# Kernel optimization log

Hardware: AMD Instinct MI355X
Metric: run time of the kernel (lower is better)

Reference implementation:

```python
import jax, jax.numpy as jnp
import numpy as np

B, S, D = 4, 2048, 1024
H = 16
HD = D // H

def setup_inputs() -> dict:
    key = jax.random.key(0)
    ks = jax.random.split(key, 6)
    std = 1.0 / np.sqrt(D)
    x = jax.random.normal(ks[0], (B, S, D), dtype=jnp.float32)
    Wq = jax.random.uniform(ks[1], (D, D), jnp.float32, -std, std)
    Wk = jax.random.uniform(ks[2], (D, D), jnp.float32, -std, std)
    Wv = jax.random.uniform(ks[3], (D, D), jnp.float32, -std, std)
    Wo = jax.random.uniform(ks[4], (D, D), jnp.float32, -std, std)
    bo = jax.random.uniform(ks[5], (D,), jnp.float32, -std, std)
    return {"x": x, "Wq": Wq, "Wk": Wk, "Wv": Wv, "Wo": Wo, "bo": bo}

def reference(x, Wq, Wk, Wv, Wo, bo):
    b, s, _ = x.shape
    # projections; torch Linear computes x @ W^T, here W stored as (d_in, d_out)... we use (D, D) applied as x @ W
    q = (x @ Wq).reshape(b, s, H, HD).transpose(0, 2, 1, 3)  # b h s hd
    k = (x @ Wk).reshape(b, s, H, HD).transpose(0, 2, 1, 3)
    v = (x @ Wv).reshape(b, s, H, HD).transpose(0, 2, 1, 3)
    scores = jnp.einsum('bhqd,bhkd->bhqk', q, k)
    causal = jnp.triu(jnp.ones((s, s), dtype=bool), k=1)
    scores = jnp.where(causal[None, None], -jnp.inf, scores)
    attn = jax.nn.softmax(scores / np.sqrt(HD), axis=-1)  # dropout=0.0 -> identity
    ctx = jnp.einsum('bhqk,bhkd->bhqd', attn, v)
    ctx = ctx.transpose(0, 2, 1, 3).reshape(b, s, D)
    return ctx @ Wo + bo
```

## Files before the change

### kernel.cpp

```cpp
#include <hip/hip_runtime.h>

typedef unsigned short u16;
typedef __bf16 bf16x8 __attribute__((ext_vector_type(8)));
typedef float f32x4 __attribute__((ext_vector_type(4)));

#define Bn 4
#define Sn 2048
#define Dn 1024
#define Hn 16
#define HDn 64

__device__ inline u16 f2bf(float f) {
  unsigned u = __builtin_bit_cast(unsigned, f);
  u += 0x7fffu + ((u >> 16) & 1u);
  return (u16)(u >> 16);
}

__device__ __forceinline__ void gl2lds16(const u16* g, u16* l) {
  __builtin_amdgcn_global_load_lds(
      (const __attribute__((address_space(1))) unsigned int*)g,
      (__attribute__((address_space(3))) unsigned int*)l, 16, 0, 0);
}

__device__ __forceinline__ float fexp2(float x) {
  return __builtin_amdgcn_exp2f(x);
}

__device__ __forceinline__ unsigned pk_bf_trunc(float lo, float hi) {
  return __builtin_amdgcn_perm(__builtin_bit_cast(unsigned, hi),
                               __builtin_bit_cast(unsigned, lo), 0x07060302u);
}

__global__ __launch_bounds__(256) void cvt4(const float* __restrict__ in,
                                            u16* __restrict__ out, int n4) {
  int i = blockIdx.x * 256 + threadIdx.x;
  if (i < n4) {
    float4 v = ((const float4*)in)[i];
    ushort4 o;
    o.x = f2bf(v.x); o.y = f2bf(v.y); o.z = f2bf(v.z); o.w = f2bf(v.w);
    ((ushort4*)out)[i] = o;
  }
}

__global__ __launch_bounds__(256) void tcvt4(const float* __restrict__ w0,
                                             const float* __restrict__ w1,
                                             const float* __restrict__ w2,
                                             const float* __restrict__ w3,
                                             u16* __restrict__ out) {
  __shared__ u16 tile[32][33];
  const float* in = (blockIdx.z == 0) ? w0 : (blockIdx.z == 1) ? w1
                   : (blockIdx.z == 2) ? w2 : w3;
  u16* dst = out + (size_t)blockIdx.z * Dn * Dn;
  int bx = blockIdx.x * 32;
  int by = blockIdx.y * 32;
  int tx = threadIdx.x & 31;
  int ty = threadIdx.x >> 5;
#pragma unroll
  for (int r = 0; r < 32; r += 8)
    tile[ty + r][tx] = f2bf(in[(size_t)(by + ty + r) * Dn + bx + tx]);
  __syncthreads();
#pragma unroll
  for (int r = 0; r < 32; r += 8)
    dst[(size_t)(bx + ty + r) * Dn + by + tx] = tile[tx][ty + r];
}

__global__ __launch_bounds__(512, 2) void gemm_qkv(const u16* __restrict__ A,
                                                   const u16* __restrict__ Bt,
                                                   u16* __restrict__ qkb,
                                                   u16* __restrict__ vt,
                                                   float qscale) {
  __shared__ __attribute__((aligned(16))) u16 S[3][3][8192];

  const int tid = threadIdx.x;
  const int lane = tid & 63;
  const int lcol = lane & 15;
  const int quad = lane >> 4;
  const int wave = tid >> 6;
  const int wr = wave >> 2;
  const int wc = wave & 3;

  const int bid = blockIdx.x;
  const int idx = bid >> 3;
  const int bm = (((bid & 7) << 3) + (idx & 7)) * 128;
  const int bn = (idx >> 3) * 256;

  const u16* srcp[3][2];
#pragma unroll
  for (int rg = 0; rg < 3; rg++) {
#pragma unroll
    for (int j = 0; j < 2; j++) {
      int o = j * 8192 + tid * 16;
      int l = o ^ (((o >> 8) & 7) << 4);
      int rho = l >> 7;
      int c2 = (l >> 1) & 63;
      int gr;
      if (rg == 0)      gr = bm + rho;
      else if (rg == 1) gr = bn + ((rho >> 5) << 6) + (rho & 31);
      else              gr = bn + ((rho >> 5) << 6) + 32 + (rho & 31);
      const u16* base = (rg == 0) ? A : Bt;
      srcp[rg][j] = base + (size_t)gr * Dn + c2;
    }
  }

  auto stg = [&](int rg, int buf, int tile) {
    if (tile >= 16) return;
    const int k0 = tile << 6;
    u16* d = &S[buf][rg][tid * 8];
    gl2lds16(srcp[rg][0] + k0, d);
    gl2lds16(srcp[rg][1] + k0, d + 4096);
  };

  f32x4 acc[4][4];
#pragma unroll
  for (int i = 0; i < 4; i++)
#pragma unroll
    for (int j = 0; j < 4; j++) acc[i][j] = (f32x4){0.f, 0.f, 0.f, 0.f};

  const int SW = (lcol & 14) << 3;
  const int cs0 = (quad * 16) ^ SW;
  const int cs1 = (64 + quad * 16) ^ SW;

  bf16x8 bk0[4], bk1[4];

#define MFMA16(a, b, c) __builtin_amdgcn_mfma_f32_16x16x32_bf16(a, b, c, 0, 0, 0)

#define ARD(D, Q, F, K)                                                      \
  (*(const bf16x8*)((const char*)&S[D][0][0] +                               \
      ((wr * 64 + (Q) * 32 + (F) * 16 + lcol) * 128 + ((K) ? cs1 : cs0))))
#define BRD(D, NI, K)                                                        \
  (*(const bf16x8*)((const char*)&S[D][1 + ((NI) >> 1)][0] +                 \
      ((wc * 32 + ((NI) & 1) * 16 + lcol) * 128 + ((K) ? cs1 : cs0))))

#define PHASE(D, Q, DO_B, STG_STMT, WAIT_STMT)                               \
  {                                                                          \
    bf16x8 a00 = ARD(D, Q, 0, 0), a01 = ARD(D, Q, 0, 1);                     \
    bf16x8 a10 = ARD(D, Q, 1, 0), a11 = ARD(D, Q, 1, 1);                     \
    if (DO_B) {                                                              \
      _Pragma("unroll") for (int ni = 0; ni < 4; ni++) {                     \
        bk0[ni] = BRD(D, ni, 0);                                             \
        bk1[ni] = BRD(D, ni, 1);                                             \
      }                                                                      \
    }                                                                        \
    STG_STMT;                                                                \
    WAIT_STMT;                                                               \
    __builtin_amdgcn_s_barrier();                                            \
    asm volatile("s_waitcnt lgkmcnt(0)" ::: "memory");                       \
    __builtin_amdgcn_sched_barrier(0);                                       \
    __builtin_amdgcn_s_setprio(1);                                           \
    _Pragma("unroll") for (int ni = 0; ni < 4; ni++) {                       \
      acc[(Q) * 2][ni] = MFMA16(a00, bk0[ni], acc[(Q) * 2][ni]);             \
      acc[(Q) * 2][ni] = MFMA16(a01, bk1[ni], acc[(Q) * 2][ni]);             \
      acc[(Q) * 2 + 1][ni] = MFMA16(a10, bk0[ni], acc[(Q) * 2 + 1][ni]);     \
      acc[(Q) * 2 + 1][ni] = MFMA16(a11, bk1[ni], acc[(Q) * 2 + 1][ni]);     \
    }                                                                        \
    __builtin_amdgcn_s_setprio(0);                                           \
    __builtin_amdgcn_s_barrier();                                            \
  }

#define TILE(D, DN, T)                                                       \
  PHASE(D, 0, 1, { stg(1, DN, (T) + 2); stg(0, DN, (T) + 2); }, )            \
  PHASE(D, 1, 0, { stg(2, DN, (T) + 2); },                                   \
        if ((T) < 14) asm volatile("s_waitcnt vmcnt(6)" ::: "memory");       \
        else if ((T) == 14) asm volatile("s_waitcnt vmcnt(0)" ::: "memory"))

  stg(1, 0, 0); stg(0, 0, 0); stg(2, 0, 0);
  stg(1, 1, 1); stg(0, 1, 1); stg(2, 1, 1);
  asm volatile("s_waitcnt vmcnt(6)" ::: "memory");
  __builtin_amdgcn_s_barrier();

#pragma unroll 1
  for (int I = 0; I < 5; ++I) {
    const int T0 = 3 * I;
    TILE(0, 2, T0)
    TILE(1, 0, T0 + 1)
    TILE(2, 1, T0 + 2)
  }
  TILE(0, 2, 15)
#undef TILE
#undef PHASE
#undef ARD
#undef BRD
#undef MFMA16

  const int rb = bm + wr * 64 + quad * 4;
  const int cb = bn + wc * 64 + lcol;
  if (bn >= 2048) {
#pragma unroll
    for (int mi = 0; mi < 4; mi++) {
#pragma unroll
      for (int ni = 0; ni < 4; ni++) {
        int row0 = rb + mi * 16;
        int s = row0 & (Sn - 1);
        int bb = row0 >> 11;
        int vcol = cb + ni * 16 - 2048;
        int bh = (bb << 4) + (vcol >> 6);
        int hd = vcol & 63;
        unsigned d0 = (unsigned)f2bf(acc[mi][ni][0]) |
                      ((unsigned)f2bf(acc[mi][ni][1]) << 16);
        unsigned d1 = (unsigned)f2bf(acc[mi][ni][2]) |
                      ((unsigned)f2bf(acc[mi][ni][3]) << 16);
        *(uint2*)(vt + ((size_t)bh * HDn + hd) * Sn + s) = (uint2){d0, d1};
      }
    }
  } else {
    const float scale = (bn < 1024) ? qscale : 1.0f;
#pragma unroll
    for (int mi = 0; mi < 4; mi++) {
#pragma unroll
      for (int ni = 0; ni < 4; ni++) {
        int row0 = rb + mi * 16;
        int col = cb + ni * 16;
#pragma unroll
        for (int r = 0; r < 4; r++)
          qkb[(size_t)(row0 + r) * 2048 + col] = f2bf(acc[mi][ni][r] * scale);
      }
    }
  }
}

__global__ __launch_bounds__(256) void gemm_out(const u16* __restrict__ A,
                                                const u16* __restrict__ Bt,
                                                float* __restrict__ Cout,
                                                const float* __restrict__ bias) {
  __shared__ __attribute__((aligned(16))) u16 As[2][2][128][32];
  __shared__ __attribute__((aligned(16))) u16 Bs[2][2][128][32];
  const int K = Dn;
  const int t = threadIdx.x;
  const int wave = t >> 6;
  const int lane = t & 63;
  const int lcol = lane & 15;
  const int quad = lane >> 4;
  const int wm = (wave >> 1) * 64;
  const int wn = (wave & 1) * 64;
  const int bm = blockIdx.y * 128;
  const int bn = blockIdx.x * 128;

  const int srow = lane >> 2;
  const int sseg = (lane & 3) * 8;
  const u16* a0p = A + (size_t)(bm + wave * 16 + srow) * K + sseg;
  const u16* a1p = a0p + (size_t)64 * K;
  const u16* b0p = Bt + (size_t)(bn + wave * 16 + srow) * K + sseg;
  const u16* b1p = b0p + (size_t)64 * K;
  u16* asl = &As[0][0][0][0] + wave * 512 + lane * 8;
  u16* bsl = &Bs[0][0][0][0] + wave * 512 + lane * 8;

  auto stage = [&](int k0, int d) {
    u16* as = asl + d * 8192;
    u16* bs = bsl + d * 8192;
    gl2lds16(a0p + k0, as);
    gl2lds16(a1p + k0, as + 2048);
    gl2lds16(a0p + k0 + 32, as + 4096);
    gl2lds16(a1p + k0 + 32, as + 6144);
    gl2lds16(b0p + k0, bs);
    gl2lds16(b1p + k0, bs + 2048);
    gl2lds16(b0p + k0 + 32, bs + 4096);
    gl2lds16(b1p + k0 + 32, bs + 6144);
  };

  f32x4 acc[4][4];
#pragma unroll
  for (int i = 0; i < 4; i++)
#pragma unroll
    for (int j = 0; j < 4; j++) acc[i][j] = (f32x4){0.f, 0.f, 0.f, 0.f};

  stage(0, 0);
  int d = 0;
  for (int k0 = 0; k0 < K; k0 += 64, d ^= 1) {
    __syncthreads();
    if (k0 + 64 < K) stage(k0 + 64, d ^ 1);
#pragma unroll
    for (int ks = 0; ks < 2; ks++) {
      bf16x8 af[4], bf[4];
#pragma unroll
      for (int mi = 0; mi < 4; mi++)
        af[mi] = *(const bf16x8*)(&As[d][ks][wm + mi * 16 + lcol][quad * 8]);
#pragma unroll
      for (int ni = 0; ni < 4; ni++)
        bf[ni] = *(const bf16x8*)(&Bs[d][ks][wn + ni * 16 + lcol][quad * 8]);
#pragma unroll
      for (int mi = 0; mi < 4; mi++)
#pragma unroll
        for (int ni = 0; ni < 4; ni++)
          acc[mi][ni] = __builtin_amdgcn_mfma_f32_16x16x32_bf16(af[mi], bf[ni], acc[mi][ni], 0, 0, 0);
    }
  }

#pragma unroll
  for (int mi = 0; mi < 4; mi++) {
#pragma unroll
    for (int ni = 0; ni < 4; ni++) {
#pragma unroll
      for (int r = 0; r < 4; r++) {
        int row = bm + wm + mi * 16 + quad * 4 + r;
        int col = bn + wn + ni * 16 + lcol;
        Cout[(size_t)row * Dn + col] = acc[mi][ni][r] + bias[col];
      }
    }
  }
}

__global__ __launch_bounds__(256, 2) void attn5(const u16* __restrict__ QK,
                                                const u16* __restrict__ Vt,
                                                u16* __restrict__ ctx) {
  __shared__ __attribute__((aligned(16))) u16 Ks2[2][64][32];
  __shared__ __attribute__((aligned(16))) u16 Vts2[2][64][32];
  __shared__ __attribute__((aligned(16))) u16 Pt[4][32][72];

  const int bh = blockIdx.x;
  const int b = bh >> 4, h = bh & 15;
  const int pair = blockIdx.y;
  const int t = threadIdx.x;
  const int w = t >> 6;
  const int lane = t & 63;
  const int lcol = lane & 15;
  const int quad = lane >> 4;
  const int qw0 = pair * 128 + w * 32;
  const int qw1 = (15 - pair) * 128 + w * 32;

  const size_t qkbase = ((size_t)b * Sn) * 2048 + h * HDn;
  const size_t obase = ((size_t)b * Sn) * Dn + h * HDn;
  const size_t vbase = ((size_t)bh * HDn) * Sn;

  bf16x8 qf[2][2][2];
#pragma unroll
  for (int si = 0; si < 2; si++) {
    const int qws = si ? qw1 : qw0;
#pragma unroll
    for (int qb = 0; qb < 2; qb++) {
      const u16* qp = QK + qkbase + (size_t)(qws + qb * 16 + lcol) * 2048 + quad * 8;
      qf[si][qb][0] = *(const bf16x8*)qp;
      qf[si][qb][1] = *(const bf16x8*)(qp + 32);
    }
  }

  f32x4 o[2][2][4];
#pragma unroll
  for (int si = 0; si < 2; si++)
#pragma unroll
    for (int qb = 0; qb < 2; qb++)
#pragma unroll
      for (int nb = 0; nb < 4; nb++) o[si][qb][nb] = (f32x4){0.f, 0.f, 0.f, 0.f};
  float lsum[2][2] = {{0.f, 0.f}, {0.f, 0.f}};

  const int srow = lane >> 2;
  const int sseg = (lane & 3) * 8;
  const u16* kp0 = QK + qkbase + 1024 + (size_t)(w * 16 + srow) * 2048 + sseg;
  const u16* vp0 = Vt + vbase + (size_t)(w * 16 + srow) * Sn + sseg;
  u16* ksl0 = &Ks2[0][0][0] + w * 512 + lane * 8;
  u16* ksl1 = ksl0 + 2048;
  u16* vsl0 = &Vts2[0][0][0] + w * 512 + lane * 8;
  u16* vsl1 = vsl0 + 2048;

  auto do_strip = [&](int si, int qw, int j0) {
    f32x4 s[4][2];
#pragma unroll
    for (int mb = 0; mb < 4; mb++) {
      bf16x8 kf0 = *(const bf16x8*)(&Ks2[0][mb * 16 + lcol][quad * 8]);
      bf16x8 kf1 = *(const bf16x8*)(&Ks2[1][mb * 16 + lcol][quad * 8]);
#pragma unroll
      for (int qb = 0; qb < 2; qb++) {
        f32x4 a = (f32x4){0.f, 0.f, 0.f, 0.f};
        a = __builtin_amdgcn_mfma_f32_16x16x32_bf16(kf0, qf[si][qb][0], a, 0, 0, 0);
        a = __builtin_amdgcn_mfma_f32_16x16x32_bf16(kf1, qf[si][qb][1], a, 0, 0, 0);
        s[mb][qb] = a;
      }
    }

    const bool needmask = (j0 + 63 > qw);
#pragma unroll
    for (int qb = 0; qb < 2; qb++) {
      const int qrow = qw + qb * 16 + lcol;
#pragma unroll
      for (int mb = 0; mb < 4; mb++) {
        float p[4];
#pragma unroll
        for (int r = 0; r < 4; r++) p[r] = fexp2(s[mb][qb][r]);
        if (needmask) {
          const int kvb = j0 + mb * 16 + quad * 4;
#pragma unroll
          for (int r = 0; r < 4; r++)
            if (kvb + r > qrow) p[r] = 0.f;
        }
        lsum[si][qb] += (p[0] + p[1]) + (p[2] + p[3]);
        unsigned d0 = pk_bf_trunc(p[0], p[1]);
        unsigned d1 = pk_bf_trunc(p[2], p[3]);
        *(uint2*)(&Pt[w][qb * 16 + lcol][mb * 16 + quad * 4]) = (uint2){d0, d1};
      }
    }

#pragma unroll
    for (int c = 0; c < 2; c++) {
      bf16x8 pf0 = *(const bf16x8*)(&Pt[w][lcol][c * 32 + quad * 8]);
      bf16x8 pf1 = *(const bf16x8*)(&Pt[w][16 + lcol][c * 32 + quad * 8]);
#pragma unroll
      for (int nb = 0; nb < 4; nb++) {
        bf16x8 vf = *(const bf16x8*)(&Vts2[c][nb * 16 + lcol][quad * 8]);
        o[si][0][nb] = __builtin_amdgcn_mfma_f32_16x16x32_bf16(vf, pf0, o[si][0][nb], 0, 0, 0);
        o[si][1][nb] = __builtin_amdgcn_mfma_f32_16x16x32_bf16(vf, pf1, o[si][1][nb], 0, 0, 0);
      }
    }
  };

  const int n_kv = (15 - pair) * 128 + 128;

  for (int j0 = 0; j0 < n_kv; j0 += 64) {
    {
      const u16* kp = kp0 + (size_t)j0 * 2048;
      gl2lds16(kp, ksl0);
      gl2lds16(kp + 32, ksl1);
      const u16* vp = vp0 + j0;
      gl2lds16(vp, vsl0);
      gl2lds16(vp + 32, vsl1);
    }
    __syncthreads();

    if (j0 <= qw1 + 31) do_strip(1, qw1, j0);
    if (j0 <= qw0 + 31) do_strip(0, qw0, j0);
    __syncthreads();
  }

#pragma unroll
  for (int si = 0; si < 2; si++) {
    const int qws = si ? qw1 : qw0;
#pragma unroll
    for (int qb = 0; qb < 2; qb++) {
      float l = lsum[si][qb];
      l += __shfl_xor(l, 16);
      l += __shfl_xor(l, 32);
      float inv = 1.0f / l;
#pragma unroll
      for (int nb = 0; nb < 4; nb++) {
        unsigned d0 = (unsigned)f2bf(o[si][qb][nb][0] * inv) |
                      ((unsigned)f2bf(o[si][qb][nb][1] * inv) << 16);
        unsigned d1 = (unsigned)f2bf(o[si][qb][nb][2] * inv) |
                      ((unsigned)f2bf(o[si][qb][nb][3] * inv) << 16);
        u16* p = ctx + obase + (size_t)(qws + qb * 16 + lcol) * Dn + nb * 16 + quad * 4;
        *(uint2*)p = (uint2){d0, d1};
      }
    }
  }
}

extern "C" void kernel_launch(void* const* d_in, const int* in_sizes, int n_in,
                              void* d_out, int out_size, void* d_ws, size_t ws_size,
                              hipStream_t stream) {
  const float* x  = (const float*)d_in[0];
  const float* Wq = (const float*)d_in[1];
  const float* Wk = (const float*)d_in[2];
  const float* Wv = (const float*)d_in[3];
  const float* Wo = (const float*)d_in[4];
  const float* bo = (const float*)d_in[5];
  float* out = (float*)d_out;

  const size_t BSD = (size_t)Bn * Sn * Dn;
  const size_t DD = (size_t)Dn * Dn;

  u16* xb    = (u16*)d_ws;
  u16* wall  = xb + BSD;
  u16* qkb   = wall + 4 * DD;
  u16* vt    = qkb + 2 * BSD;
  u16* cb    = vt + BSD;

  cvt4<<<(int)(BSD / 4 / 256), 256, 0, stream>>>(x, xb, (int)(BSD / 4));
  tcvt4<<<dim3(Dn / 32, Dn / 32, 4), 256, 0, stream>>>(Wq, Wk, Wv, Wo, wall);

  gemm_qkv<<<dim3(768), 512, 0, stream>>>(xb, wall, qkb, vt,
                                          0.125f * 1.44269504f);

  attn5<<<dim3(Bn * Hn, 8), 256, 0, stream>>>(qkb, vt, cb);

  gemm_out<<<dim3(Dn / 128, (Bn * Sn) / 128), 256, 0, stream>>>(cb, wall + 3 * DD, out, bo);
}
```

Before: 247.5 us.

## Port output GEMM to triple-buffered swizzled pipeline and restructure QKV k-loop

The output projection GEMM moves from a simple double-buffered 128x128 kernel to the same 512-thread, triple-buffered, XOR-swizzled LDS pipeline used by the QKV GEMM, with a grouped block mapping and hoisted bias loads. The shared k-loop is rewritten so each 64-wide K tile issues all stage loads up front and runs one merged MFMA phase per tile instead of two half-phases, cutting barriers per tile from four to one. The aim is better latency hiding, fewer bank conflicts and fewer synchronisations. The cost is more register pressure, and the output GEMM now launches only 256 blocks of 128x256 tiles, which may underfill the GPU.

```diff
diff --git a/kernel.cpp b/kernel.cpp
--- a/kernel.cpp
+++ b/kernel.cpp
@@ -64,6 +64,81 @@
     dst[(size_t)(bx + ty + r) * Dn + by + tx] = tile[tx][ty + r];
 }
 
+#define MFMA16(a, b, c) __builtin_amdgcn_mfma_f32_16x16x32_bf16(a, b, c, 0, 0, 0)
+
+#define SRCP_INIT(APTR, BPTR)                                                \
+  const u16* srcp[3][2];                                                     \
+  _Pragma("unroll") for (int rg = 0; rg < 3; rg++) {                         \
+    _Pragma("unroll") for (int j = 0; j < 2; j++) {                          \
+      int o = j * 8192 + tid * 16;                                           \
+      int l = o ^ (((o >> 8) & 7) << 4);                                     \
+      int rho = l >> 7;                                                      \
+      int c2 = (l >> 1) & 63;                                                \
+      int gr;                                                                \
+      if (rg == 0)      gr = bm + rho;                                       \
+      else if (rg == 1) gr = bn + ((rho >> 5) << 6) + (rho & 31);            \
+      else              gr = bn + ((rho >> 5) << 6) + 32 + (rho & 31);       \
+      const u16* base = (rg == 0) ? (APTR) : (BPTR);                         \
+      srcp[rg][j] = base + (size_t)gr * Dn + c2;                             \
+    }                                                                        \
+  }
+
+#define ARD(D, Q, F, K)                                                      \
+  (*(const bf16x8*)((const char*)&S[D][0][0] +                               \
+      ((wr * 64 + (Q) * 32 + (F) * 16 + lcol) * 128 + ((K) ? cs1 : cs0))))
+#define BRD(D, NI, K)                                                        \
+  (*(const bf16x8*)((const char*)&S[D][1 + ((NI) >> 1)][0] +                 \
+      ((wc * 32 + ((NI) & 1) * 16 + lcol) * 128 + ((K) ? cs1 : cs0))))
+
+#define VM6 asm volatile("s_waitcnt vmcnt(6)" ::: "memory")
+#define VM0 asm volatile("s_waitcnt vmcnt(0)" ::: "memory")
+
+#define KTILE(D, DN, T, WAIT)                                                \
+  {                                                                          \
+    stg(0, DN, (T) + 2); stg(1, DN, (T) + 2); stg(2, DN, (T) + 2);           \
+    bf16x8 a00 = ARD(D, 0, 0, 0), a01 = ARD(D, 0, 0, 1);                     \
+    bf16x8 a10 = ARD(D, 0, 1, 0), a11 = ARD(D, 0, 1, 1);                     \
+    bf16x8 a20 = ARD(D, 1, 0, 0), a21 = ARD(D, 1, 0, 1);                     \
+    bf16x8 a30 = ARD(D, 1, 1, 0), a31 = ARD(D, 1, 1, 1);                     \
+    bf16x8 bk0[4], bk1[4];                                                   \
+    _Pragma("unroll") for (int ni = 0; ni < 4; ni++) {                       \
+      bk0[ni] = BRD(D, ni, 0); bk1[ni] = BRD(D, ni, 1);                      \
+    }                                                                        \
+    asm volatile("s_waitcnt lgkmcnt(0)" ::: "memory");                       \
+    __builtin_amdgcn_sched_barrier(0);                                       \
+    __builtin_amdgcn_s_setprio(1);                                           \
+    _Pragma("unroll") for (int ni = 0; ni < 4; ni++) {                       \
+      acc[0][ni] = MFMA16(a00, bk0[ni], acc[0][ni]);                         \
+      acc[1][ni] = MFMA16(a10, bk0[ni], acc[1][ni]);                         \
+      acc[2][ni] = MFMA16(a20, bk0[ni], acc[2][ni]);                         \
+      acc[3][ni] = MFMA16(a30, bk0[ni], acc[3][ni]);                         \
+    }                                                                        \
+    _Pragma("unroll") for (int ni = 0; ni < 4; ni++) {                       \
+      acc[0][ni] = MFMA16(a01, bk1[ni], acc[0][ni]);                         \
+      acc[1][ni] = MFMA16(a11, bk1[ni], acc[1][ni]);                         \
+      acc[2][ni] = MFMA16(a21, bk1[ni], acc[2][ni]);                         \
+      acc[3][ni] = MFMA16(a31, bk1[ni], acc[3][ni]);                         \
+    }                                                                        \
+    __builtin_amdgcn_s_setprio(0);                                           \
+    WAIT;                                                                    \
+    __builtin_amdgcn_s_barrier();                                            \
+    __builtin_amdgcn_sched_barrier(0);                                       \
+  }
+
+#define KLOOP                                                                \
+  stg(0, 0, 0); stg(1, 0, 0); stg(2, 0, 0);                                  \
+  stg(0, 1, 1); stg(1, 1, 1); stg(2, 1, 1);                                  \
+  VM6;                                                                       \
+  __builtin_amdgcn_s_barrier();                                              \
+  __builtin_amdgcn_sched_barrier(0);                                         \
+  _Pragma("unroll 1") for (int I = 0; I < 5; ++I) {                          \
+    const int T0 = 3 * I;                                                    \
+    KTILE(0, 2, T0, VM6)                                                     \
+    KTILE(1, 0, T0 + 1, VM6)                                                 \
+    KTILE(2, 1, T0 + 2, if (I == 4) { VM0; } else { VM6; })                  \
+  }                                                                          \
+  KTILE(0, 2, 15, )
+
 __global__ __launch_bounds__(512, 2) void gemm_qkv(const u16* __restrict__ A,
                                                    const u16* __restrict__ Bt,
                                                    u16* __restrict__ qkb,
@@ -84,23 +159,7 @@
   const int bm = (((bid & 7) << 3) + (idx & 7)) * 128;
   const int bn = (idx >> 3) * 256;
 
-  const u16* srcp[3][2];
-#pragma unroll
-  for (int rg = 0; rg < 3; rg++) {
-#pragma unroll
-    for (int j = 0; j < 2; j++) {
-      int o = j * 8192 + tid * 16;
-      int l = o ^ (((o >> 8) & 7) << 4);
-      int rho = l >> 7;
-      int c2 = (l >> 1) & 63;
-      int gr;
-      if (rg == 0)      gr = bm + rho;
-      else if (rg == 1) gr = bn + ((rho >> 5) << 6) + (rho & 31);
-      else              gr = bn + ((rho >> 5) << 6) + 32 + (rho & 31);
-      const u16* base = (rg == 0) ? A : Bt;
-      srcp[rg][j] = base + (size_t)gr * Dn + c2;
-    }
-  }
+  SRCP_INIT(A, Bt)
 
   auto stg = [&](int rg, int buf, int tile) {
     if (tile >= 16) return;
@@ -120,67 +179,7 @@
   const int cs0 = (quad * 16) ^ SW;
   const int cs1 = (64 + quad * 16) ^ SW;
 
-  bf16x8 bk0[4], bk1[4];
-
-#define MFMA16(a, b, c) __builtin_amdgcn_mfma_f32_16x16x32_bf16(a, b, c, 0, 0, 0)
-
-#define ARD(D, Q, F, K)                                                      \
-  (*(const bf16x8*)((const char*)&S[D][0][0] +                               \
-      ((wr * 64 + (Q) * 32 + (F) * 16 + lcol) * 128 + ((K) ? cs1 : cs0))))
-#define BRD(D, NI, K)                                                        \
-  (*(const bf16x8*)((const char*)&S[D][1 + ((NI) >> 1)][0] +                 \
-      ((wc * 32 + ((NI) & 1) * 16 + lcol) * 128 + ((K) ? cs1 : cs0))))
-
-#define PHASE(D, Q, DO_B, STG_STMT, WAIT_STMT)                               \
-  {                                                                          \
-    bf16x8 a00 = ARD(D, Q, 0, 0), a01 = ARD(D, Q, 0, 1);                     \
-    bf16x8 a10 = ARD(D, Q, 1, 0), a11 = ARD(D, Q, 1, 1);                     \
-    if (DO_B) {                                                              \
-      _Pragma("unroll") for (int ni = 0; ni < 4; ni++) {                     \
-        bk0[ni] = BRD(D, ni, 0);                                             \
-        bk1[ni] = BRD(D, ni, 1);                                             \
-      }                                                                      \
-    }                                                                        \
-    STG_STMT;                                                                \
-    WAIT_STMT;                                                               \
-    __builtin_amdgcn_s_barrier();                                            \
-    asm volatile("s_waitcnt lgkmcnt(0)" ::: "memory");                       \
-    __builtin_amdgcn_sched_barrier(0);                                       \
-    __builtin_amdgcn_s_setprio(1);                                           \
-    _Pragma("unroll") for (int ni = 0; ni < 4; ni++) {                       \
-      acc[(Q) * 2][ni] = MFMA16(a00, bk0[ni], acc[(Q) * 2][ni]);             \
-      acc[(Q) * 2][ni] = MFMA16(a01, bk1[ni], acc[(Q) * 2][ni]);             \
-      acc[(Q) * 2 + 1][ni] = MFMA16(a10, bk0[ni], acc[(Q) * 2 + 1][ni]);     \
-      acc[(Q) * 2 + 1][ni] = MFMA16(a11, bk1[ni], acc[(Q) * 2 + 1][ni]);     \
-    }                                                                        \
-    __builtin_amdgcn_s_setprio(0);                                           \
-    __builtin_amdgcn_s_barrier();                                            \
-  }
-
-#define TILE(D, DN, T)                                                       \
-  PHASE(D, 0, 1, { stg(1, DN, (T) + 2); stg(0, DN, (T) + 2); }, )            \
-  PHASE(D, 1, 0, { stg(2, DN, (T) + 2); },                                   \
-        if ((T) < 14) asm volatile("s_waitcnt vmcnt(6)" ::: "memory");       \
-        else if ((T) == 14) asm volatile("s_waitcnt vmcnt(0)" ::: "memory"))
-
-  stg(1, 0, 0); stg(0, 0, 0); stg(2, 0, 0);
-  stg(1, 1, 1); stg(0, 1, 1); stg(2, 1, 1);
-  asm volatile("s_waitcnt vmcnt(6)" ::: "memory");
-  __builtin_amdgcn_s_barrier();
-
-#pragma unroll 1
-  for (int I = 0; I < 5; ++I) {
-    const int T0 = 3 * I;
-    TILE(0, 2, T0)
-    TILE(1, 0, T0 + 1)
-    TILE(2, 1, T0 + 2)
-  }
-  TILE(0, 2, 15)
-#undef TILE
-#undef PHASE
-#undef ARD
-#undef BRD
-#undef MFMA16
+  KLOOP
 
   const int rb = bm + wr * 64 + quad * 4;
   const int cb = bn + wc * 64 + lcol;
@@ -218,43 +217,33 @@
   }
 }
 
-__global__ __launch_bounds__(256) void gemm_out(const u16* __restrict__ A,
-                                                const u16* __restrict__ Bt,
-                                                float* __restrict__ Cout,
-                                                const float* __restrict__ bias) {
-  __shared__ __attribute__((aligned(16))) u16 As[2][2][128][32];
-  __shared__ __attribute__((aligned(16))) u16 Bs[2][2][128][32];
-  const int K = Dn;
-  const int t = threadIdx.x;
-  const int wave = t >> 6;
-  const int lane = t & 63;
+__global__ __launch_bounds__(512, 2) void gemm_out(const u16* __restrict__ A,
+                                                   const u16* __restrict__ Bt,
+                                                   float* __restrict__ Cout,
+                                                   const float* __restrict__ bias) {
+  __shared__ __attribute__((aligned(16))) u16 S[3][3][8192];
+
+  const int tid = threadIdx.x;
+  const int lane = tid & 63;
   const int lcol = lane & 15;
   const int quad = lane >> 4;
-  const int wm = (wave >> 1) * 64;
-  const int wn = (wave & 1) * 64;
-  const int bm = blockIdx.y * 128;
-  const int bn = blockIdx.x * 128;
-
-  const int srow = lane >> 2;
-  const int sseg = (lane & 3) * 8;
-  const u16* a0p = A + (size_t)(bm + wave * 16 + srow) * K + sseg;
-  const u16* a1p = a0p + (size_t)64 * K;
-  const u16* b0p = Bt + (size_t)(bn + wave * 16 + srow) * K + sseg;
-  const u16* b1p = b0p + (size_t)64 * K;
-  u16* asl = &As[0][0][0][0] + wave * 512 + lane * 8;
-  u16* bsl = &Bs[0][0][0][0] + wave * 512 + lane * 8;
-
-  auto stage = [&](int k0, int d) {
-    u16* as = asl + d * 8192;
-    u16* bs = bsl + d * 8192;
-    gl2lds16(a0p + k0, as);
-    gl2lds16(a1p + k0, as + 2048);
-    gl2lds16(a0p + k0 + 32, as + 4096);
-    gl2lds16(a1p + k0 + 32, as + 6144);
-    gl2lds16(b0p + k0, bs);
-    gl2lds16(b1p + k0, bs + 2048);
-    gl2lds16(b0p + k0 + 32, bs + 4096);
-    gl2lds16(b1p + k0 + 32, bs + 6144);
+  const int wave = tid >> 6;
+  const int wr = wave >> 2;
+  const int wc = wave & 3;
+
+  const int bid = blockIdx.x;
+  const int idx = bid >> 3;
+  const int bm = (((bid & 7) << 3) + (idx & 7)) * 128;
+  const int bn = (idx >> 3) * 256;
+
+  SRCP_INIT(A, Bt)
+
+  auto stg = [&](int rg, int buf, int tile) {
+    if (tile >= 16) return;
+    const int k0 = tile << 6;
+    u16* d = &S[buf][rg][tid * 8];
+    gl2lds16(srcp[rg][0] + k0, d);
+    gl2lds16(srcp[rg][1] + k0, d + 4096);
   };
 
   f32x4 acc[4][4];
@@ -263,38 +252,26 @@
 #pragma unroll
     for (int j = 0; j < 4; j++) acc[i][j] = (f32x4){0.f, 0.f, 0.f, 0.f};
 
-  stage(0, 0);
-  int d = 0;
-  for (int k0 = 0; k0 < K; k0 += 64, d ^= 1) {
-    __syncthreads();
-    if (k0 + 64 < K) stage(k0 + 64, d ^ 1);
-#pragma unroll
-    for (int ks = 0; ks < 2; ks++) {
-      bf16x8 af[4], bf[4];
-#pragma unroll
-      for (int mi = 0; mi < 4; mi++)
-        af[mi] = *(const bf16x8*)(&As[d][ks][wm + mi * 16 + lcol][quad * 8]);
-#pragma unroll
-      for (int ni = 0; ni < 4; ni++)
-        bf[ni] = *(const bf16x8*)(&Bs[d][ks][wn + ni * 16 + lcol][quad * 8]);
-#pragma unroll
-      for (int mi = 0; mi < 4; mi++)
-#pragma unroll
-        for (int ni = 0; ni < 4; ni++)
-          acc[mi][ni] = __builtin_amdgcn_mfma_f32_16x16x32_bf16(af[mi], bf[ni], acc[mi][ni], 0, 0, 0);
-    }
-  }
-
+  const int SW = (lcol & 14) << 3;
+  const int cs0 = (quad * 16) ^ SW;
+  const int cs1 = (64 + quad * 16) ^ SW;
+
+  KLOOP
+
+  const int rb = bm + wr * 64 + quad * 4;
+  const int cb = bn + wc * 64 + lcol;
+  float bv[4];
+#pragma unroll
+  for (int ni = 0; ni < 4; ni++) bv[ni] = bias[cb + ni * 16];
 #pragma unroll
   for (int mi = 0; mi < 4; mi++) {
 #pragma unroll
     for (int ni = 0; ni < 4; ni++) {
-#pragma unroll
-      for (int r = 0; r < 4; r++) {
-        int row = bm + wm + mi * 16 + quad * 4 + r;
-        int col = bn + wn + ni * 16 + lcol;
-        Cout[(size_t)row * Dn + col] = acc[mi][ni][r] + bias[col];
-      }
+      int row0 = rb + mi * 16;
+      int col = cb + ni * 16;
+#pragma unroll
+      for (int r = 0; r < 4; r++)
+        Cout[(size_t)(row0 + r) * Dn + col] = acc[mi][ni][r] + bv[ni];
     }
   }
 }
@@ -469,5 +446,5 @@
 
   attn5<<<dim3(Bn * Hn, 8), 256, 0, stream>>>(qkb, vt, cb);
 
-  gemm_out<<<dim3(Dn / 128, (Bn * Sn) / 128), 256, 0, stream>>>(cb, wall + 3 * DD, out, bo);
-}
+  gemm_out<<<dim3(256), 512, 0, stream>>>(cb, wall + 3 * DD, out, bo);
+}
```

Result: faster. 225.3 us (-8.9%).
